# Performance work log

Measured on AMD Instinct MI355X. Metric: run time of the kernel, lower is better.

Reference implementation:

```python
import jax, jax.numpy as jnp
import numpy as np

D_HEAD = 64  # d_adapter // n_heads with n_heads=1

def setup_inputs() -> dict:
    key = jax.random.key(0)
    ks = jax.random.split(key, 7)
    L, B, S, D = 8, 2, 4096, 2048
    N, Ds, Da = 128, 1024, 64
    g = 0.1  # xavier gain used in init (only affects scale; use plain normals scaled similarly)
    return {
        "hidden": jax.random.normal(ks[0], (L, B, S, D), jnp.float32),
        "bank": jax.random.normal(ks[1], (B, N, Ds), jnp.float32),
        "Wq": jax.random.normal(ks[2], (L, Da, D), jnp.float32) * (g / np.sqrt(D)),
        "Wk": jax.random.normal(ks[3], (L, Da, Ds), jnp.float32) * (g / np.sqrt(Ds)),
        "Wv": jax.random.normal(ks[4], (L, Da, Ds), jnp.float32) * (g / np.sqrt(Ds)),
        "Wo": jax.random.normal(ks[5], (L, D, Da), jnp.float32) * (g / np.sqrt(Da)),
        "gates": jnp.full((L,), -2.0, jnp.float32),
    }

def reference(hidden, bank, Wq, Wk, Wv, Wo, gates):
    # hidden: (L,B,S,D) per-layer hidden states; bank: (B,N,Ds) shared summary bank
    h = hidden.astype(jnp.float32)
    bk = bank.astype(jnp.float32)
    Q = jnp.einsum('lbsd,lad->lbsa', h, Wq)        # (L,B,S,Da)
    K = jnp.einsum('bnc,lac->lbna', bk, Wk)        # (L,B,N,Da)
    V = jnp.einsum('bnc,lac->lbna', bk, Wv)        # (L,B,N,Da)
    scale = 1.0 / jnp.sqrt(jnp.asarray(D_HEAD, jnp.float32))
    scores = jnp.einsum('lbsa,lbna->lbsn', Q, K) * scale
    attn = jax.nn.softmax(scores, axis=-1)          # (L,B,S,N)
    attn_out = jnp.einsum('lbsn,lbna->lbsa', attn, V)
    resid = jnp.einsum('lbsa,lda->lbsd', attn_out, Wo)
    gate = jax.nn.sigmoid(gates)[:, None, None, None]
    return hidden + (gate * resid).astype(hidden.dtype)
```

## Files before the change

kernel.cpp:

```cpp
#include <hip/hip_runtime.h>
#include <cstdint>
#include <cstddef>


typedef __attribute__((ext_vector_type(8))) short short8;
typedef __attribute__((ext_vector_type(4))) float f32x4;
typedef __attribute__((ext_vector_type(4))) unsigned short u16x4;

#define MFMA16(a, b, c) __builtin_amdgcn_mfma_f32_16x16x32_bf16((a), (b), (c), 0, 0, 0)

__device__ __forceinline__ unsigned short f2bf(float f) {
  unsigned int x = __builtin_bit_cast(unsigned int, f);
  x += 0x7fffu + ((x >> 16) & 1u);
  return (unsigned short)(x >> 16);
}
__device__ __forceinline__ float bf2f(unsigned short u) {
  return __builtin_bit_cast(float, (unsigned int)u << 16);
}
__device__ __forceinline__ short8 cvt8v(f32x4 a, f32x4 b) {
  short8 r;
  r[0] = (short)f2bf(a[0]); r[1] = (short)f2bf(a[1]);
  r[2] = (short)f2bf(a[2]); r[3] = (short)f2bf(a[3]);
  r[4] = (short)f2bf(b[0]); r[5] = (short)f2bf(b[1]);
  r[6] = (short)f2bf(b[2]); r[7] = (short)f2bf(b[3]);
  return r;
}
__device__ __forceinline__ short8 ld_cvt8(const float* p) {
  f32x4 v0 = *(const f32x4*)p, v1 = *(const f32x4*)(p + 4);
  return cvt8v(v0, v1);
}
__device__ __forceinline__ u16x4 pack4(f32x4 v) {
  u16x4 r;
  r[0] = f2bf(v[0]); r[1] = f2bf(v[1]); r[2] = f2bf(v[2]); r[3] = f2bf(v[3]);
  return r;
}

__global__ __launch_bounds__(64)
void pre_kv_kernel(const float* __restrict__ bank,
                   const float* __restrict__ Wk,
                   const float* __restrict__ Wv,
                   unsigned short* __restrict__ KF, unsigned short* __restrict__ VF) {
  int bid = blockIdx.x;
  int at = bid & 3, nt = (bid >> 2) & 7, kv = (bid >> 5) & 1;
  int b = (bid >> 6) & 1, l = bid >> 7;
  int lane = threadIdx.x & 63;
  int lo = lane & 15, hi = lane >> 4;
  const float* W  = (kv ? Wv : Wk) + (size_t)l * 65536;
  const float* bk = bank + (size_t)b * 131072;
  int lbq = l * 2 + b;
  f32x4 acc = (f32x4){0.f, 0.f, 0.f, 0.f};
  for (int ks = 0; ks < 32; ++ks) {
    short8 A = ld_cvt8(bk + (nt * 16 + lo) * 1024 + ks * 32 + hi * 8);
    short8 B = ld_cvt8(W + (at * 16 + lo) * 1024 + ks * 32 + hi * 8);
    acc = MFMA16(A, B, acc);
  }
  for (int r = 0; r < 4; ++r) {
    int n = nt * 16 + hi * 4 + r;
    int a = at * 16 + lo;
    unsigned short v = f2bf(acc[r]);
    if (kv == 0) {
      int idx = ((lbq * 8 + (n >> 4)) * 2 + (a >> 5)) * 512 +
                (((a >> 3) & 3) * 16 + (n & 15)) * 8 + (a & 7);
      KF[idx] = v;
    } else {
      int idx = ((lbq * 4 + (a >> 4)) * 4 + (n >> 5)) * 512 +
                (((n >> 3) & 3) * 16 + (a & 15)) * 8 + (n & 7);
      VF[idx] = v;
    }
  }
}

__global__ void pre_frag_kernel(const float* __restrict__ Wq, const float* __restrict__ Wo,
                                unsigned short* __restrict__ WqF, unsigned short* __restrict__ WoF) {
  int idx = blockIdx.x * 256 + threadIdx.x;
  if (idx < 131072) {
    int t = idx;
    int lane = t & 63, ks = (t >> 6) & 63, at = (t >> 12) & 3, l = t >> 14;
    int a = at * 16 + (lane & 15), d = ks * 32 + (lane >> 4) * 8;
    *(short8*)(WqF + (size_t)t * 8) = ld_cvt8(Wq + ((size_t)(l * 64 + a)) * 2048 + d);
  } else {
    int t = idx - 131072;
    int lane = t & 63, ks = (t >> 6) & 1, dt = (t >> 7) & 127, l = t >> 14;
    int d = dt * 16 + (lane & 15), a = ks * 32 + (lane >> 4) * 8;
    *(short8*)(WoF + (size_t)t * 8) = ld_cvt8(Wo + ((size_t)(l * 2048 + d)) * 64 + a);
  }
}

__global__ __launch_bounds__(256, 8)
void adapter_main(const float* __restrict__ hidden,
                  const unsigned short* __restrict__ KF, const unsigned short* __restrict__ VF,
                  const unsigned short* __restrict__ WqF, const unsigned short* __restrict__ WoF,
                  const float* __restrict__ gates, float* __restrict__ out) {
  __shared__ __align__(16) char smem[12800];
  float* qsc = (float*)(smem + 4096);
  float* scb = (float*)smem;
  unsigned short* Pb = (unsigned short*)(smem + 8192);
  float* aob = (float*)smem;

  int bid0 = blockIdx.x;
  int bid = (bid0 & 7) * 512 + (bid0 >> 3);
  int st = bid & 255, b = (bid >> 8) & 1, l = bid >> 9;
  int tid = threadIdx.x, wave = tid >> 6, lane = tid & 63;
  int lo = lane & 15, hi = lane >> 4;
  int l32 = lane & 31, lh = lane >> 5;
  size_t hbase = ((size_t)(l * 2 + b) * 4096 + st * 16) * 2048;
  const char* hby = (const char*)(hidden + hbase);
  float gate = 1.0f / (1.0f + __expf(-gates[l]));
  int lb = l * 2 + b;
  int at = wave;

  f32x4 sreg[2];
  f32x4 qacc = (f32x4){0.f, 0.f, 0.f, 0.f};
  {
    const unsigned short* wqb = WqF + ((size_t)(l * 4 + at) * 64) * 512 + lane * 8;

#define LOADC(c)                                                             \
    _Pragma("unroll")                                                        \
    for (int s2 = 0; s2 < 2; ++s2) {                                         \
      int row = (s2 * 4 + wave) * 2 + lh;                                    \
      sreg[s2] = *(const f32x4*)(hby + (size_t)row * 8192 + (size_t)(c) * 512 + l32 * 16); \
    }
#define WRITEC(c)                                                            \
    _Pragma("unroll")                                                        \
    for (int s2 = 0; s2 < 2; ++s2) {                                         \
      int row = (s2 * 4 + wave) * 2 + lh;                                    \
      u16x4 pk = pack4(sreg[s2]);                                            \
      *(u16x4*)(smem + (1 - ((c) & 1)) * 4096 + row * 256 + ((l32 * 8) ^ ((row & 7) << 4))) = pk; \
    }

    LOADC(0); WRITEC(0);
    #pragma unroll 1
    for (int c = 0; c < 16; ++c) {
      __syncthreads();
      if (c < 15) LOADC(c + 1);
      const char* rb = smem + (1 - (c & 1)) * 4096 + lo * 256;
      int sw = (lo & 7) << 4;
      #pragma unroll
      for (int ks = 0; ks < 4; ++ks) {
        short8 A = *(const short8*)(rb + ((ks * 64 + hi * 16) ^ sw));
        short8 B = *(const short8*)(wqb + (size_t)(c * 4 + ks) * 512);
        qacc = MFMA16(A, B, qacc);
      }
      if (c < 15) WRITEC(c + 1);
    }
#undef LOADC
#undef WRITEC
  }

  #pragma unroll
  for (int r = 0; r < 4; ++r)
    qsc[(hi * 4 + r) * 66 + at * 16 + lo] = qacc[r] * 0.125f;
  __syncthreads();

  {
    short8 afrag[2];
    #pragma unroll
    for (int ks = 0; ks < 2; ++ks) {
      const float* qp = qsc + lo * 66 + ks * 32 + hi * 8;
      afrag[ks] = cvt8v(*(const f32x4*)qp, *(const f32x4*)(qp + 4));
    }
    __syncthreads();
    #pragma unroll
    for (int i = 0; i < 2; ++i) {
      int nt = wave * 2 + i;
      f32x4 acc = (f32x4){0.f, 0.f, 0.f, 0.f};
      const unsigned short* kf = KF + ((size_t)(lb * 8 + nt) * 2) * 512 + lane * 8;
      acc = MFMA16(afrag[0], *(const short8*)(kf), acc);
      acc = MFMA16(afrag[1], *(const short8*)(kf + 512), acc);
      #pragma unroll
      for (int r = 0; r < 4; ++r)
        scb[(hi * 4 + r) * 128 + nt * 16 + lo] = acc[r];
    }
  }
  __syncthreads();

  {
    int row = wave * 4 + hi;
    const float* sp = scb + row * 128 + lo * 8;
    f32x4 v0 = *(const f32x4*)sp, v1 = *(const f32x4*)(sp + 4);
    float m = fmaxf(fmaxf(fmaxf(v0[0], v0[1]), fmaxf(v0[2], v0[3])),
                    fmaxf(fmaxf(v1[0], v1[1]), fmaxf(v1[2], v1[3])));
    m = fmaxf(m, __shfl_xor(m, 1)); m = fmaxf(m, __shfl_xor(m, 2));
    m = fmaxf(m, __shfl_xor(m, 4)); m = fmaxf(m, __shfl_xor(m, 8));
    f32x4 e0, e1; float s = 0.f;
    #pragma unroll
    for (int j = 0; j < 4; ++j) { e0[j] = __expf(v0[j] - m); s += e0[j]; }
    #pragma unroll
    for (int j = 0; j < 4; ++j) { e1[j] = __expf(v1[j] - m); s += e1[j]; }
    s += __shfl_xor(s, 1); s += __shfl_xor(s, 2);
    s += __shfl_xor(s, 4); s += __shfl_xor(s, 8);
    float inv = 1.0f / s;
    #pragma unroll
    for (int j = 0; j < 4; ++j) { e0[j] *= inv; e1[j] *= inv; }
    *(short8*)((char*)Pb + row * 272 + lo * 16) = cvt8v(e0, e1);
  }
  __syncthreads();

  {
    short8 pfrag[4];
    #pragma unroll
    for (int ks = 0; ks < 4; ++ks)
      pfrag[ks] = *(const short8*)((const char*)Pb + lo * 272 + ks * 64 + hi * 16);
    const unsigned short* vf = VF + ((size_t)(lb * 4 + at) * 4) * 512 + lane * 8;
    f32x4 a = (f32x4){0.f, 0.f, 0.f, 0.f};
    #pragma unroll
    for (int ks = 0; ks < 4; ++ks)
      a = MFMA16(pfrag[ks], *(const short8*)(vf + (size_t)ks * 512), a);
    #pragma unroll
    for (int r = 0; r < 4; ++r)
      aob[(hi * 4 + r) * 66 + at * 16 + lo] = a[r];
  }
  __syncthreads();

  {
    short8 bfrag[2];
    #pragma unroll
    for (int ks = 0; ks < 2; ++ks) {
      const float* ap2 = aob + lo * 66 + ks * 32 + hi * 8;
      bfrag[ks] = cvt8v(*(const f32x4*)ap2, *(const f32x4*)(ap2 + 4));
    }
    float* ob = out + hbase;
    #pragma unroll 1
    for (int c = 0; c < 16; ++c) {
      char* resb = smem + 4352 + (c & 1) * 4224;
      #pragma unroll
      for (int j = 0; j < 2; ++j) {
        int dtl = wave * 2 + j;
        int dt = c * 8 + dtl;
        const unsigned short* wo = WoF + ((size_t)(l * 128 + dt) * 2) * 512 + lane * 8;
        short8 A0 = *(const short8*)(wo);
        short8 A1 = *(const short8*)(wo + 512);
        f32x4 acc = (f32x4){0.f, 0.f, 0.f, 0.f};
        acc = MFMA16(A0, bfrag[0], acc);
        acc = MFMA16(A1, bfrag[1], acc);
        *(u16x4*)(resb + lo * 264 + dtl * 32 + hi * 8) = pack4(acc);
      }
      __syncthreads();
      #pragma unroll
      for (int i2 = 0; i2 < 2; ++i2) {
        int row = (i2 * 4 + wave) * 2 + lh;
        size_t off = (size_t)row * 8192 + (size_t)c * 512 + l32 * 16;
        f32x4 hv = *(const f32x4*)(hby + off);
        u16x4 rv = *(const u16x4*)(resb + row * 264 + l32 * 8);
        f32x4 o;
        #pragma unroll
        for (int r = 0; r < 4; ++r) o[r] = hv[r] + gate * bf2f(rv[r]);
        __builtin_nontemporal_store(o, (f32x4*)((char*)ob + off));
      }
    }
  }
}

extern "C" void kernel_launch(void* const* d_in, const int* in_sizes, int n_in,
                              void* d_out, int out_size, void* d_ws, size_t ws_size,
                              hipStream_t stream) {
  const float* hidden = (const float*)d_in[0];
  const float* bank   = (const float*)d_in[1];
  const float* Wq     = (const float*)d_in[2];
  const float* Wk     = (const float*)d_in[3];
  const float* Wv     = (const float*)d_in[4];
  const float* Wo     = (const float*)d_in[5];
  const float* gates  = (const float*)d_in[6];
  float* out = (float*)d_out;

  char* ws = (char*)d_ws;
  unsigned short* KF  = (unsigned short*)(ws);
  unsigned short* VF  = (unsigned short*)(ws + 262144);
  unsigned short* WqF = (unsigned short*)(ws + 524288);
  unsigned short* WoF = (unsigned short*)(ws + 2621440);

  pre_kv_kernel<<<1024, 64, 0, stream>>>(bank, Wk, Wv, KF, VF);
  pre_frag_kernel<<<1024, 256, 0, stream>>>(Wq, Wo, WqF, WoF);
  adapter_main<<<4096, 256, 0, stream>>>(hidden, KF, VF, WqF, WoF, gates, out);
}
```

Before: 338.8 us.

## Stream hidden tiles via global_load_lds DMA and software-pipeline Q and output phases

Replaces the register-staged hidden load, bf16 pack and LDS write in the Q projection with direct global-to-LDS 16-byte loads into a 4-deep fp32 ring. Waits use manual vmcnt counts and raw s_barrier, and each A fragment is converted to bf16 when it is read from LDS. The output phase prefetches the next chunk's Wo fragments and hidden values into registers ahead of the MFMA and store work. Shared memory grows and the occupancy hint drops from 8 to 6 blocks per CU, trading occupancy for latency hiding through explicit pipelining. The hand-tuned waitcnt counts risk being wrong if the compiler adds or reorders memory ops.

```diff
diff --git a/kernel.cpp b/kernel.cpp
--- a/kernel.cpp
+++ b/kernel.cpp
@@ -33,6 +33,12 @@
   u16x4 r;
   r[0] = f2bf(v[0]); r[1] = f2bf(v[1]); r[2] = f2bf(v[2]); r[3] = f2bf(v[3]);
   return r;
+}
+__device__ __forceinline__ void gload_lds16(const void* g, void* l) {
+  typedef __attribute__((address_space(1))) const unsigned int gu32;
+  typedef __attribute__((address_space(3))) unsigned int lu32;
+  __builtin_amdgcn_global_load_lds((gu32*)(const unsigned int*)g,
+                                   (lu32*)(unsigned int*)l, 16, 0, 0);
 }
 
 __global__ __launch_bounds__(64)
@@ -86,16 +92,16 @@
   }
 }
 
-__global__ __launch_bounds__(256, 8)
+__global__ __launch_bounds__(256, 6)
 void adapter_main(const float* __restrict__ hidden,
                   const unsigned short* __restrict__ KF, const unsigned short* __restrict__ VF,
                   const unsigned short* __restrict__ WqF, const unsigned short* __restrict__ WoF,
                   const float* __restrict__ gates, float* __restrict__ out) {
-  __shared__ __align__(16) char smem[12800];
-  float* qsc = (float*)(smem + 4096);
+  __shared__ __align__(16) char smem[20608];
   float* scb = (float*)smem;
-  unsigned short* Pb = (unsigned short*)(smem + 8192);
-  float* aob = (float*)smem;
+  unsigned short* Pb = (unsigned short*)(smem + 8448);
+  float* qsc = (float*)(smem + 16384);
+  float* aob = (float*)(smem + 16384);
 
   int bid0 = blockIdx.x;
   int bid = (bid0 & 7) * 512 + (bid0 >> 3);
@@ -108,43 +114,60 @@
   float gate = 1.0f / (1.0f + __expf(-gates[l]));
   int lb = l * 2 + b;
   int at = wave;
-
-  f32x4 sreg[2];
+  char* stg = smem;
+
   f32x4 qacc = (f32x4){0.f, 0.f, 0.f, 0.f};
   {
     const unsigned short* wqb = WqF + ((size_t)(l * 4 + at) * 64) * 512 + lane * 8;
-
-#define LOADC(c)                                                             \
-    _Pragma("unroll")                                                        \
-    for (int s2 = 0; s2 < 2; ++s2) {                                         \
-      int row = (s2 * 4 + wave) * 2 + lh;                                    \
-      sreg[s2] = *(const f32x4*)(hby + (size_t)row * 8192 + (size_t)(c) * 512 + l32 * 16); \
-    }
-#define WRITEC(c)                                                            \
-    _Pragma("unroll")                                                        \
-    for (int s2 = 0; s2 < 2; ++s2) {                                         \
-      int row = (s2 * 4 + wave) * 2 + lh;                                    \
-      u16x4 pk = pack4(sreg[s2]);                                            \
-      *(u16x4*)(smem + (1 - ((c) & 1)) * 4096 + row * 256 + ((l32 * 8) ^ ((row & 7) << 4))) = pk; \
-    }
-
-    LOADC(0); WRITEC(0);
+    int rowg = wave * 4 + hi;
+    rowg = wave * 4 + (lane >> 4) - hi + hi;
+    int r4 = lane >> 4;
+    rowg = wave * 4 + r4;
+    size_t gsw = (size_t)(((lane & 15) * 16) ^ ((rowg & 7) << 5));
+    const char* gsrc = hby + (size_t)rowg * 8192 + gsw;
+    char* ldst = stg + wave * 1024;
+    int swr = (lo & 7) << 5;
+
+#define DMA1(c) gload_lds16(gsrc + (size_t)(c) * 256, ldst + ((c) & 3) * 4096)
+#define BLD(c, dst)                                                          \
+    do {                                                                     \
+      dst##0 = *(const short8*)(wqb + (size_t)(2 * (c)) * 512);              \
+      dst##1 = *(const short8*)(wqb + (size_t)(2 * (c) + 1) * 512);          \
+    } while (0)
+#define P1BODY(c, Br)                                                        \
+    do {                                                                     \
+      const char* rb = stg + ((c) & 3) * 4096 + lo * 256;                    \
+      int y0 = (hi * 32) ^ swr, y1 = (128 + hi * 32) ^ swr;                  \
+      short8 A0 = cvt8v(*(const f32x4*)(rb + y0), *(const f32x4*)(rb + y0 + 16)); \
+      short8 A1 = cvt8v(*(const f32x4*)(rb + y1), *(const f32x4*)(rb + y1 + 16)); \
+      qacc = MFMA16(A0, Br##0, qacc);                                        \
+      qacc = MFMA16(A1, Br##1, qacc);                                        \
+    } while (0)
+
+    short8 Be0, Be1, Bo0, Bo1;
+    DMA1(0); DMA1(1); BLD(0, Be);
     #pragma unroll 1
-    for (int c = 0; c < 16; ++c) {
-      __syncthreads();
-      if (c < 15) LOADC(c + 1);
-      const char* rb = smem + (1 - (c & 1)) * 4096 + lo * 256;
-      int sw = (lo & 7) << 4;
-      #pragma unroll
-      for (int ks = 0; ks < 4; ++ks) {
-        short8 A = *(const short8*)(rb + ((ks * 64 + hi * 16) ^ sw));
-        short8 B = *(const short8*)(wqb + (size_t)(c * 4 + ks) * 512);
-        qacc = MFMA16(A, B, qacc);
+    for (int p = 0; p < 16; ++p) {
+      int c = 2 * p;
+      if (p < 15) { DMA1(c + 2); }
+      BLD(c + 1, Bo);
+      if (p < 15) { asm volatile("s_waitcnt vmcnt(6)" ::: "memory"); }
+      else        { asm volatile("s_waitcnt vmcnt(5)" ::: "memory"); }
+      __builtin_amdgcn_s_barrier();
+      P1BODY(c, Be);
+      if (p < 15) {
+        DMA1(c + 3);
+        BLD(c + 2, Be);
+        asm volatile("s_waitcnt vmcnt(6)" ::: "memory");
+      } else {
+        asm volatile("s_waitcnt vmcnt(2)" ::: "memory");
       }
-      if (c < 15) WRITEC(c + 1);
-    }
-#undef LOADC
-#undef WRITEC
+      __builtin_amdgcn_s_barrier();
+      P1BODY(c + 1, Bo);
+    }
+#undef DMA1
+#undef BLD
+#undef P1BODY
   }
 
   #pragma unroll
@@ -159,7 +182,6 @@
       const float* qp = qsc + lo * 66 + ks * 32 + hi * 8;
       afrag[ks] = cvt8v(*(const f32x4*)qp, *(const f32x4*)(qp + 4));
     }
-    __syncthreads();
     #pragma unroll
     for (int i = 0; i < 2; ++i) {
       int nt = wave * 2 + i;
@@ -219,35 +241,54 @@
       const float* ap2 = aob + lo * 66 + ks * 32 + hi * 8;
       bfrag[ks] = cvt8v(*(const f32x4*)ap2, *(const f32x4*)(ap2 + 4));
     }
-    float* ob = out + hbase;
+    const unsigned short* wobase = WoF + (size_t)l * 131072 + lane * 8;
+    char* ob = (char*)(out + hbase);
+    int hr0 = wave * 2 + lh, hr1 = 8 + wave * 2 + lh;
+
+#define P5LOAD(c, W0a, W0b, W1a, W1b, H0, H1)                                \
+    do {                                                                     \
+      const unsigned short* wo = wobase + (size_t)((c) * 8 + wave * 2) * 1024; \
+      W0a = *(const short8*)(wo);        W0b = *(const short8*)(wo + 512);   \
+      W1a = *(const short8*)(wo + 1024); W1b = *(const short8*)(wo + 1536);  \
+      H0 = *(const f32x4*)(hby + (size_t)hr0 * 8192 + (c) * 512 + l32 * 16); \
+      H1 = *(const f32x4*)(hby + (size_t)hr1 * 8192 + (c) * 512 + l32 * 16); \
+    } while (0)
+#define P5BODY(c, W0a, W0b, W1a, W1b, H0, H1)                                \
+    do {                                                                     \
+      char* rs = smem + ((c) & 1) * 4224;                                    \
+      f32x4 a0 = (f32x4){0.f, 0.f, 0.f, 0.f};                                \
+      a0 = MFMA16(W0a, bfrag[0], a0); a0 = MFMA16(W0b, bfrag[1], a0);        \
+      f32x4 a1 = (f32x4){0.f, 0.f, 0.f, 0.f};                                \
+      a1 = MFMA16(W1a, bfrag[0], a1); a1 = MFMA16(W1b, bfrag[1], a1);        \
+      *(u16x4*)(rs + lo * 264 + (wave * 2) * 32 + hi * 8) = pack4(a0);       \
+      *(u16x4*)(rs + lo * 264 + (wave * 2 + 1) * 32 + hi * 8) = pack4(a1);   \
+      asm volatile("s_waitcnt lgkmcnt(0)" ::: "memory");                     \
+      __builtin_amdgcn_s_barrier();                                          \
+      u16x4 rv0 = *(const u16x4*)(rs + hr0 * 264 + l32 * 8);                 \
+      u16x4 rv1 = *(const u16x4*)(rs + hr1 * 264 + l32 * 8);                 \
+      f32x4 o0, o1;                                                          \
+      _Pragma("unroll")                                                      \
+      for (int r = 0; r < 4; ++r) {                                          \
+        o0[r] = H0[r] + gate * bf2f(rv0[r]);                                 \
+        o1[r] = H1[r] + gate * bf2f(rv1[r]);                                 \
+      }                                                                      \
+      __builtin_nontemporal_store(o0, (f32x4*)(ob + (size_t)hr0 * 8192 + (c) * 512 + l32 * 16)); \
+      __builtin_nontemporal_store(o1, (f32x4*)(ob + (size_t)hr1 * 8192 + (c) * 512 + l32 * 16)); \
+    } while (0)
+
+    short8 wE0a, wE0b, wE1a, wE1b, wO0a, wO0b, wO1a, wO1b;
+    f32x4 hE0, hE1, hO0, hO1;
+    P5LOAD(0, wE0a, wE0b, wE1a, wE1b, hE0, hE1);
     #pragma unroll 1
-    for (int c = 0; c < 16; ++c) {
-      char* resb = smem + 4352 + (c & 1) * 4224;
-      #pragma unroll
-      for (int j = 0; j < 2; ++j) {
-        int dtl = wave * 2 + j;
-        int dt = c * 8 + dtl;
-        const unsigned short* wo = WoF + ((size_t)(l * 128 + dt) * 2) * 512 + lane * 8;
-        short8 A0 = *(const short8*)(wo);
-        short8 A1 = *(const short8*)(wo + 512);
-        f32x4 acc = (f32x4){0.f, 0.f, 0.f, 0.f};
-        acc = MFMA16(A0, bfrag[0], acc);
-        acc = MFMA16(A1, bfrag[1], acc);
-        *(u16x4*)(resb + lo * 264 + dtl * 32 + hi * 8) = pack4(acc);
-      }
-      __syncthreads();
-      #pragma unroll
-      for (int i2 = 0; i2 < 2; ++i2) {
-        int row = (i2 * 4 + wave) * 2 + lh;
-        size_t off = (size_t)row * 8192 + (size_t)c * 512 + l32 * 16;
-        f32x4 hv = *(const f32x4*)(hby + off);
-        u16x4 rv = *(const u16x4*)(resb + row * 264 + l32 * 8);
-        f32x4 o;
-        #pragma unroll
-        for (int r = 0; r < 4; ++r) o[r] = hv[r] + gate * bf2f(rv[r]);
-        __builtin_nontemporal_store(o, (f32x4*)((char*)ob + off));
-      }
-    }
+    for (int p = 0; p < 8; ++p) {
+      int c = 2 * p;
+      P5LOAD(c + 1, wO0a, wO0b, wO1a, wO1b, hO0, hO1);
+      P5BODY(c, wE0a, wE0b, wE1a, wE1b, hE0, hE1);
+      if (p < 7) P5LOAD(c + 2, wE0a, wE0b, wE1a, wE1b, hE0, hE1);
+      P5BODY(c + 1, wO0a, wO0b, wO1a, wO1b, hO0, hO1);
+    }
+#undef P5LOAD
+#undef P5BODY
   }
 }
 
```

New measurement: 395.9 us. 16.9% more time.

## Process 32 sequence rows per 512-thread block to reuse Wq/Wo fragments

Applied to the files above, without the earlier changes.

Doubles the row tile from 16 to 32 rows per block, using 8 waves split into two M-tiles. Each Wo fragment load now feeds two MFMA pairs, which halves Wo/Wq/K/V fragment traffic per row and halves the grid size. The cost is more LDS per block (about 34KB), an extra barrier per output chunk, and possibly lower occupancy, since the 512,8 launch bound may not be met. The epilogue now does full-row 1KB-contiguous accesses per wave.

```diff
diff --git a/kernel.cpp b/kernel.cpp
--- a/kernel.cpp
+++ b/kernel.cpp
@@ -86,46 +86,49 @@
   }
 }
 
-__global__ __launch_bounds__(256, 8)
+__global__ __launch_bounds__(512, 8)
 void adapter_main(const float* __restrict__ hidden,
                   const unsigned short* __restrict__ KF, const unsigned short* __restrict__ VF,
                   const unsigned short* __restrict__ WqF, const unsigned short* __restrict__ WoF,
                   const float* __restrict__ gates, float* __restrict__ out) {
-  __shared__ __align__(16) char smem[12800];
-  float* qsc = (float*)(smem + 4096);
-  float* scb = (float*)smem;
-  unsigned short* Pb = (unsigned short*)(smem + 8192);
-  float* aob = (float*)smem;
+  __shared__ __align__(16) char smem[34048];
+  float* qsc = (float*)smem;
+  unsigned short* Pb = (unsigned short*)(smem + 8448);
+  float* scb = (float*)(smem + 17152);
+  float* aob = (float*)(smem + 17152);
+  char* resb = smem + 17152;
 
   int bid0 = blockIdx.x;
-  int bid = (bid0 & 7) * 512 + (bid0 >> 3);
-  int st = bid & 255, b = (bid >> 8) & 1, l = bid >> 9;
+  int bid = (bid0 & 7) * 256 + (bid0 >> 3);
+  int st = bid & 127, b = (bid >> 7) & 1, l = bid >> 8;
   int tid = threadIdx.x, wave = tid >> 6, lane = tid & 63;
   int lo = lane & 15, hi = lane >> 4;
   int l32 = lane & 31, lh = lane >> 5;
-  size_t hbase = ((size_t)(l * 2 + b) * 4096 + st * 16) * 2048;
+  int mt = wave >> 2, at = wave & 3;
+  size_t hbase = ((size_t)(l * 2 + b) * 4096 + st * 32) * 2048;
   const char* hby = (const char*)(hidden + hbase);
   float gate = 1.0f / (1.0f + __expf(-gates[l]));
   int lb = l * 2 + b;
-  int at = wave;
 
   f32x4 sreg[2];
   f32x4 qacc = (f32x4){0.f, 0.f, 0.f, 0.f};
   {
     const unsigned short* wqb = WqF + ((size_t)(l * 4 + at) * 64) * 512 + lane * 8;
+    int arow = mt * 16 + lo;
+    int sw = (arow & 7) << 4;
 
 #define LOADC(c)                                                             \
     _Pragma("unroll")                                                        \
     for (int s2 = 0; s2 < 2; ++s2) {                                         \
-      int row = (s2 * 4 + wave) * 2 + lh;                                    \
+      int row = (s2 * 8 + wave) * 2 + lh;                                    \
       sreg[s2] = *(const f32x4*)(hby + (size_t)row * 8192 + (size_t)(c) * 512 + l32 * 16); \
     }
 #define WRITEC(c)                                                            \
     _Pragma("unroll")                                                        \
     for (int s2 = 0; s2 < 2; ++s2) {                                         \
-      int row = (s2 * 4 + wave) * 2 + lh;                                    \
+      int row = (s2 * 8 + wave) * 2 + lh;                                    \
       u16x4 pk = pack4(sreg[s2]);                                            \
-      *(u16x4*)(smem + (1 - ((c) & 1)) * 4096 + row * 256 + ((l32 * 8) ^ ((row & 7) << 4))) = pk; \
+      *(u16x4*)(smem + ((c) & 1) * 8192 + row * 256 + ((l32 * 8) ^ ((row & 7) << 4))) = pk; \
     }
 
     LOADC(0); WRITEC(0);
@@ -133,8 +136,7 @@
     for (int c = 0; c < 16; ++c) {
       __syncthreads();
       if (c < 15) LOADC(c + 1);
-      const char* rb = smem + (1 - (c & 1)) * 4096 + lo * 256;
-      int sw = (lo & 7) << 4;
+      const char* rb = smem + (c & 1) * 8192 + arow * 256;
       #pragma unroll
       for (int ks = 0; ks < 4; ++ks) {
         short8 A = *(const short8*)(rb + ((ks * 64 + hi * 16) ^ sw));
@@ -146,37 +148,37 @@
 #undef LOADC
 #undef WRITEC
   }
+  __syncthreads();
 
   #pragma unroll
   for (int r = 0; r < 4; ++r)
-    qsc[(hi * 4 + r) * 66 + at * 16 + lo] = qacc[r] * 0.125f;
+    qsc[(mt * 16 + hi * 4 + r) * 66 + at * 16 + lo] = qacc[r] * 0.125f;
   __syncthreads();
 
   {
     short8 afrag[2];
     #pragma unroll
     for (int ks = 0; ks < 2; ++ks) {
-      const float* qp = qsc + lo * 66 + ks * 32 + hi * 8;
+      const float* qp = qsc + (mt * 16 + lo) * 66 + ks * 32 + hi * 8;
       afrag[ks] = cvt8v(*(const f32x4*)qp, *(const f32x4*)(qp + 4));
     }
-    __syncthreads();
     #pragma unroll
     for (int i = 0; i < 2; ++i) {
-      int nt = wave * 2 + i;
+      int nt = at * 2 + i;
       f32x4 acc = (f32x4){0.f, 0.f, 0.f, 0.f};
       const unsigned short* kf = KF + ((size_t)(lb * 8 + nt) * 2) * 512 + lane * 8;
       acc = MFMA16(afrag[0], *(const short8*)(kf), acc);
       acc = MFMA16(afrag[1], *(const short8*)(kf + 512), acc);
       #pragma unroll
       for (int r = 0; r < 4; ++r)
-        scb[(hi * 4 + r) * 128 + nt * 16 + lo] = acc[r];
+        scb[(mt * 16 + hi * 4 + r) * 132 + nt * 16 + lo] = acc[r];
     }
   }
   __syncthreads();
 
   {
     int row = wave * 4 + hi;
-    const float* sp = scb + row * 128 + lo * 8;
+    const float* sp = scb + row * 132 + lo * 8;
     f32x4 v0 = *(const f32x4*)sp, v1 = *(const f32x4*)(sp + 4);
     float m = fmaxf(fmaxf(fmaxf(v0[0], v0[1]), fmaxf(v0[2], v0[3])),
                     fmaxf(fmaxf(v1[0], v1[1]), fmaxf(v1[2], v1[3])));
@@ -200,7 +202,7 @@
     short8 pfrag[4];
     #pragma unroll
     for (int ks = 0; ks < 4; ++ks)
-      pfrag[ks] = *(const short8*)((const char*)Pb + lo * 272 + ks * 64 + hi * 16);
+      pfrag[ks] = *(const short8*)((const char*)Pb + (mt * 16 + lo) * 272 + ks * 64 + hi * 16);
     const unsigned short* vf = VF + ((size_t)(lb * 4 + at) * 4) * 512 + lane * 8;
     f32x4 a = (f32x4){0.f, 0.f, 0.f, 0.f};
     #pragma unroll
@@ -208,45 +210,51 @@
       a = MFMA16(pfrag[ks], *(const short8*)(vf + (size_t)ks * 512), a);
     #pragma unroll
     for (int r = 0; r < 4; ++r)
-      aob[(hi * 4 + r) * 66 + at * 16 + lo] = a[r];
-  }
-  __syncthreads();
-
-  {
-    short8 bfrag[2];
-    #pragma unroll
-    for (int ks = 0; ks < 2; ++ks) {
-      const float* ap2 = aob + lo * 66 + ks * 32 + hi * 8;
-      bfrag[ks] = cvt8v(*(const f32x4*)ap2, *(const f32x4*)(ap2 + 4));
-    }
-    float* ob = out + hbase;
+      aob[(mt * 16 + hi * 4 + r) * 66 + at * 16 + lo] = a[r];
+  }
+  __syncthreads();
+
+  {
+    short8 bfrag[2][2];
+    #pragma unroll
+    for (int m2 = 0; m2 < 2; ++m2)
+      #pragma unroll
+      for (int ks = 0; ks < 2; ++ks) {
+        const float* ap2 = aob + (m2 * 16 + lo) * 66 + ks * 32 + hi * 8;
+        bfrag[m2][ks] = cvt8v(*(const f32x4*)ap2, *(const f32x4*)(ap2 + 4));
+      }
+    __syncthreads();
+    char* ob = (char*)(out + hbase);
     #pragma unroll 1
-    for (int c = 0; c < 16; ++c) {
-      char* resb = smem + 4352 + (c & 1) * 4224;
+    for (int c = 0; c < 8; ++c) {
       #pragma unroll
       for (int j = 0; j < 2; ++j) {
         int dtl = wave * 2 + j;
-        int dt = c * 8 + dtl;
+        int dt = c * 16 + dtl;
         const unsigned short* wo = WoF + ((size_t)(l * 128 + dt) * 2) * 512 + lane * 8;
         short8 A0 = *(const short8*)(wo);
         short8 A1 = *(const short8*)(wo + 512);
-        f32x4 acc = (f32x4){0.f, 0.f, 0.f, 0.f};
-        acc = MFMA16(A0, bfrag[0], acc);
-        acc = MFMA16(A1, bfrag[1], acc);
-        *(u16x4*)(resb + lo * 264 + dtl * 32 + hi * 8) = pack4(acc);
+        #pragma unroll
+        for (int m2 = 0; m2 < 2; ++m2) {
+          f32x4 acc = (f32x4){0.f, 0.f, 0.f, 0.f};
+          acc = MFMA16(A0, bfrag[m2][0], acc);
+          acc = MFMA16(A1, bfrag[m2][1], acc);
+          *(u16x4*)(resb + (m2 * 16 + lo) * 520 + dtl * 32 + hi * 8) = pack4(acc);
+        }
       }
       __syncthreads();
       #pragma unroll
-      for (int i2 = 0; i2 < 2; ++i2) {
-        int row = (i2 * 4 + wave) * 2 + lh;
-        size_t off = (size_t)row * 8192 + (size_t)c * 512 + l32 * 16;
+      for (int i2 = 0; i2 < 4; ++i2) {
+        int row = i2 * 8 + wave;
+        size_t off = (size_t)row * 8192 + (size_t)c * 1024 + lane * 16;
         f32x4 hv = *(const f32x4*)(hby + off);
-        u16x4 rv = *(const u16x4*)(resb + row * 264 + l32 * 8);
+        u16x4 rv = *(const u16x4*)(resb + row * 520 + lane * 8);
         f32x4 o;
         #pragma unroll
         for (int r = 0; r < 4; ++r) o[r] = hv[r] + gate * bf2f(rv[r]);
-        __builtin_nontemporal_store(o, (f32x4*)((char*)ob + off));
-      }
+        __builtin_nontemporal_store(o, (f32x4*)(ob + off));
+      }
+      __syncthreads();
     }
   }
 }
@@ -271,5 +279,5 @@
 
   pre_kv_kernel<<<1024, 64, 0, stream>>>(bank, Wk, Wv, KF, VF);
   pre_frag_kernel<<<1024, 256, 0, stream>>>(Wq, Wo, WqF, WoF);
-  adapter_main<<<4096, 256, 0, stream>>>(hidden, KF, VF, WqF, WoF, gates, out);
-}
+  adapter_main<<<2048, 512, 0, stream>>>(hidden, KF, VF, WqF, WoF, gates, out);
+}
```

New measurement: 331.6 us. -2.1%, faster.
